# Optimization experiments

Measured on AMD Instinct MI355X. Metric: run time of the kernel, lower is better.

Reference implementation:

```python
import jax, jax.numpy as jnp
import numpy as np

H = 32        # query heads
D = 128       # head size
HID = H * D   # 4096
B = 4
S = 1024
T = B * S
NSLOTS = 16384
THETA = 10000.0


def _rope(x, cos, sin):
    # x: [T, ..., D]; cos/sin: [T, D//2] -> broadcast over head dims
    half = x.shape[-1] // 2
    while cos.ndim < x.ndim:
        cos = cos[:, None]
        sin = sin[:, None]
    x1, x2 = x[..., :half], x[..., half:]
    return jnp.concatenate([x1 * cos - x2 * sin, x2 * cos + x1 * sin], axis=-1)


def setup_inputs() -> dict:
    key = jax.random.key(0)
    ks = jax.random.split(key, 6)
    hidden_states = jax.random.normal(ks[0], (T, HID), jnp.float32)
    # rotary tables from real positions (repeat per sequence in the batch)
    pos = jnp.tile(jnp.arange(S, dtype=jnp.float32), B)          # [T]
    inv_freq = 1.0 / (THETA ** (jnp.arange(0, D, 2, dtype=jnp.float32) / D))  # [D/2]
    ang = pos[:, None] * inv_freq[None, :]                        # [T, D/2]
    cos, sin = jnp.cos(ang), jnp.sin(ang)
    qkv_w = jax.random.normal(ks[1], (HID, HID + 2 * D), jnp.float32) * 0.02
    qkv_b = jax.random.normal(ks[2], (HID + 2 * D,), jnp.float32) * 0.02
    dense_w = jax.random.normal(ks[3], (HID, HID), jnp.float32) * 0.02
    dense_b = jax.random.normal(ks[4], (HID,), jnp.float32) * 0.02
    k_cache = jnp.zeros((NSLOTS, D), jnp.float32)
    v_cache = jnp.zeros((NSLOTS, D), jnp.float32)
    slots = jnp.arange(T, dtype=jnp.int32)
    return {"hidden_states": hidden_states, "cos": cos, "sin": sin,
            "k_cache": k_cache, "v_cache": v_cache,
            "qkv_w": qkv_w, "qkv_b": qkv_b, "dense_w": dense_w,
            "dense_b": dense_b, "slots": slots, "batch_size": B}


def reference(hidden_states, cos, sin, k_cache, v_cache,
              qkv_w, qkv_b, dense_w, dense_b, slots, batch_size):
    scale = D ** -0.5
    qkv = hidden_states @ qkv_w + qkv_b                  # [T, H*D + 2D]
    q = qkv[:, :HID].reshape(T, H, D)                    # [T,H,D]
    kv = qkv[:, HID:].reshape(T, 2, D)                   # MQA: 1 kv head
    k, v = kv[:, 0], kv[:, 1]                            # [T,D]
    q = _rope(q, cos, sin)
    k = _rope(k, cos, sin)
    # KV-cache scatter store
    k_cache = k_cache.at[slots].set(k)
    v_cache = v_cache.at[slots].set(v)
    # prefill varlen causal attention (uniform lengths -> [B,S] layout)
    qb = q.reshape(batch_size, S, H, D)
    kb = k.reshape(batch_size, S, D)
    vb = v.reshape(batch_size, S, D)
    scores = jnp.einsum('bqhd,bkd->bhqk', qb, kb) * scale
    causal = jnp.tril(jnp.ones((S, S), bool))
    scores = jnp.where(causal[None, None], scores, jnp.float32(-1e30))
    probs = jax.nn.softmax(scores, axis=-1)
    attn = jnp.einsum('bhqk,bkd->bqhd', probs, vb).reshape(T, HID)
    out = attn @ dense_w + dense_b                       # [T, HID]
    return out, k_cache, v_cache
```

## Files before the change

kernel.cpp:

```cpp
#include <hip/hip_runtime.h>

#define H_   32
#define D_   128
#define HID_ 4096
#define B_   4
#define S_   1024
#define T_   4096
#define NSLOTS_ 16384
#define NQKV_ 4352

typedef __attribute__((ext_vector_type(8))) __bf16 bf16x8;
typedef __attribute__((ext_vector_type(4))) __bf16 bf16x4;
typedef __attribute__((ext_vector_type(4))) float  f32x4;

__device__ __forceinline__ void gld_lds16(const __bf16* g, __bf16* l)
{
    __builtin_amdgcn_global_load_lds(
        (const __attribute__((address_space(1))) void*)g,
        (__attribute__((address_space(3))) void*)l, 16, 0, 0);
}

__device__ __forceinline__ bf16x8 ds_read_b128a(const __bf16* p)
{
    bf16x8 r;
    unsigned a = (unsigned)(size_t)(const __attribute__((address_space(3))) __bf16*)p;
    asm volatile("ds_read_b128 %0, %1" : "=&v"(r) : "v"(a));
    return r;
}

__global__ __launch_bounds__(256) void cast_bf16_kernel(
    const float* __restrict__ in, __bf16* __restrict__ out, int n4)
{
    int i = blockIdx.x * 256 + threadIdx.x;
    if (i < n4) {
        f32x4 v = ((const f32x4*)in)[i];
        bf16x4 o;
        o[0] = (__bf16)v[0]; o[1] = (__bf16)v[1];
        o[2] = (__bf16)v[2]; o[3] = (__bf16)v[3];
        ((bf16x4*)out)[i] = o;
    }
}

__global__ __launch_bounds__(256) void transpose_cast_kernel(
    const float* __restrict__ in, __bf16* __restrict__ out, int R, int C)
{
    __shared__ float tile[32][33];
    int c0 = blockIdx.x * 32, r0 = blockIdx.y * 32;
    int tx = threadIdx.x;
    int ty = threadIdx.y;
#pragma unroll
    for (int j = 0; j < 32; j += 8)
        tile[ty + j][tx] = in[(size_t)(r0 + ty + j) * C + c0 + tx];
    __syncthreads();
#pragma unroll
    for (int j = 0; j < 32; j += 8)
        out[(size_t)(c0 + ty + j) * R + r0 + tx] = (__bf16)tile[tx][ty + j];
}


#define SB()    __builtin_amdgcn_sched_barrier(0)
#define BAR()   __builtin_amdgcn_s_barrier()
#define LGKM0() asm volatile("s_waitcnt lgkmcnt(0)" ::: "memory")

#define LOAD_A(MH, KK)                                                          \
    _Pragma("unroll")                                                           \
    for (int m = 0; m < 4; ++m)                                                 \
        afr[m] = ds_read_b128a(&lds[buf][KK][(wm * 128 + ((MH)*4 + m) * 16 + col) * 32 + pbE]);

#define MFMA_QUAD(MH, KK)                                                       \
    __builtin_amdgcn_s_setprio(1);                                              \
    _Pragma("unroll")                                                           \
    for (int m = 0; m < 4; ++m) {                                               \
        _Pragma("unroll")                                                       \
        for (int n = 0; n < 4; ++n)                                             \
            acc[(MH)*4 + m][n] = __builtin_amdgcn_mfma_f32_16x16x32_bf16(       \
                afr[m], bfr[KK][n], acc[(MH)*4 + m][n], 0, 0, 0);               \
    }                                                                           \
    __builtin_amdgcn_s_setprio(0);

__global__ __launch_bounds__(512, 2) void gemm256_kernel(
    const __bf16* __restrict__ A, const __bf16* __restrict__ Bt,
    const float* __restrict__ bias, float* __restrict__ C,
    int M, int N, int K)
{
    __shared__ __bf16 lds[2][4][8192];

    const int tid  = threadIdx.x;
    const int lane = tid & 63;
    const int wave = tid >> 6;
    const int wm   = wave >> 2;
    const int wn   = wave & 3;
    const int col  = lane & 15;
    const int quad = lane >> 4;
    const int pbE  = (quad ^ ((lane >> 1) & 3)) * 8;
    const int bm   = blockIdx.y * 256;
    const int bn   = blockIdx.x * 256;
    const int nk   = K >> 6;
    const int nitems = nk << 2;

    const int sR = wave * 32 + (lane >> 2);
    const int sb = ((lane & 3) ^ ((lane >> 3) & 3)) * 8;
    const __bf16* gA = A  + (size_t)(bm + sR) * K + sb;
    const __bf16* gB = Bt + (size_t)(bn + sR) * K + sb;

    f32x4 acc[8][4];
#pragma unroll
    for (int m = 0; m < 8; ++m)
#pragma unroll
        for (int n = 0; n < 4; ++n)
#pragma unroll
            for (int r = 0; r < 4; ++r) acc[m][n][r] = 0.f;

    auto stage = [&](int idx) {
        if (idx >= nitems) return;
        const int j   = idx >> 2;
        const int sel = idx & 3;
        const int reg = sel ^ 2;
        const __bf16* g = (sel & 2) ? gA : gB;
        const size_t koff = (size_t)j * 64 + (size_t)(sel & 1) * 32;
        __bf16* l = &lds[j & 1][reg][wave * 1024];
        gld_lds16(g + koff, l);
        gld_lds16(g + koff + (size_t)16 * K, l + 512);
    };

    stage(0); stage(1); stage(2); stage(3);
    asm volatile("s_waitcnt vmcnt(4)" ::: "memory");
    stage(4); stage(5); stage(6);
    asm volatile("s_waitcnt vmcnt(6)" ::: "memory");
    BAR();
    SB();

    for (int k = 0; k < nk; ++k) {
        const int buf = k & 1;
        bf16x8 bfr[2][4];
        bf16x8 afr[4];

#pragma unroll
        for (int kk = 0; kk < 2; ++kk)
#pragma unroll
            for (int n = 0; n < 4; ++n)
                bfr[kk][n] = ds_read_b128a(&lds[buf][2 + kk][(wn * 64 + n * 16 + col) * 32 + pbE]);
        LOAD_A(0, 0)
        stage(4 * k + 7);
        SB(); BAR(); LGKM0(); SB();
        MFMA_QUAD(0, 0)
        SB(); BAR(); SB();

        LOAD_A(1, 0)
        stage(4 * k + 8);
        SB(); BAR(); LGKM0(); SB();
        MFMA_QUAD(1, 0)
        SB(); BAR(); SB();

        LOAD_A(0, 1)
        stage(4 * k + 9);
        SB(); BAR(); LGKM0(); SB();
        MFMA_QUAD(0, 1)
        SB(); BAR(); SB();

        LOAD_A(1, 1)
        stage(4 * k + 10);
        SB(); BAR(); LGKM0(); SB();
        MFMA_QUAD(1, 1)
        SB();
        if (k < nk - 2) asm volatile("s_waitcnt vmcnt(6)" ::: "memory");
        else            asm volatile("s_waitcnt vmcnt(0)" ::: "memory");
        BAR();
        SB();
    }

#pragma unroll
    for (int m = 0; m < 8; ++m) {
#pragma unroll
        for (int n = 0; n < 4; ++n) {
            const int r0 = bm + wm * 128 + m * 16 + quad * 4;
            const int c0 = bn + wn * 64 + n * 16 + col;
            const float bv = bias[c0];
#pragma unroll
            for (int r = 0; r < 4; ++r)
                C[(size_t)(r0 + r) * N + c0] = acc[m][n][r] + bv;
        }
    }
}

__global__ __launch_bounds__(256) void rope_scatter_kernel(
    const float* __restrict__ qkv, const float* __restrict__ cosb,
    const float* __restrict__ sinb, const int* __restrict__ slots,
    __bf16* __restrict__ q16, __bf16* __restrict__ k16, __bf16* __restrict__ v16,
    float* __restrict__ kcache, float* __restrict__ vcache)
{
    const int t = blockIdx.x;
    const int tid = threadIdx.x;
    const float* row = qkv + (size_t)t * NQKV_;
    const float* cr = cosb + (size_t)t * 64;
    const float* sr = sinb + (size_t)t * 64;
    const int slot = slots[t];

#pragma unroll
    for (int i = 0; i < 8; ++i) {
        int p = tid + 256 * i;
        int h = p >> 6;
        int d = p & 63;
        float x1 = row[h * 128 + d];
        float x2 = row[h * 128 + 64 + d];
        float c = cr[d], s = sr[d];
        q16[(size_t)t * HID_ + h * 128 + d]      = (__bf16)(x1 * c - x2 * s);
        q16[(size_t)t * HID_ + h * 128 + 64 + d] = (__bf16)(x2 * c + x1 * s);
    }
    if (tid < 64) {
        int d = tid;
        float x1 = row[HID_ + d];
        float x2 = row[HID_ + 64 + d];
        float c = cr[d], s = sr[d];
        float o1 = x1 * c - x2 * s;
        float o2 = x2 * c + x1 * s;
        kcache[(size_t)slot * D_ + d]      = o1;
        kcache[(size_t)slot * D_ + 64 + d] = o2;
        k16[(size_t)t * D_ + d]      = (__bf16)o1;
        k16[(size_t)t * D_ + 64 + d] = (__bf16)o2;
    }
    if (tid < 128) {
        float v = row[HID_ + 128 + tid];
        vcache[(size_t)slot * D_ + tid] = v;
        v16[(size_t)t * D_ + tid] = (__bf16)v;
    }
}

__global__ __launch_bounds__(256) void attn_kernel(
    const __bf16* __restrict__ Q, const __bf16* __restrict__ Kc,
    const __bf16* __restrict__ Vc, __bf16* __restrict__ O)
{
    __shared__ __bf16 sK[64][136];
    __shared__ __bf16 sVt[128][72];
    __shared__ __bf16 sP[4][32][72];

    const int h  = blockIdx.y;
    const int b  = blockIdx.z;
    const int tid = threadIdx.x, lane = tid & 63, wave = tid >> 6;
    const int col = lane & 15, quad = lane >> 4;
    const int tbase = b * S_;
    const float scale = 0.08838834764831845f;

    for (int half = 0; half < 2; ++half) {
        const int qt = half ? (7 - blockIdx.x) : blockIdx.x;
        const int qb = qt * 128;

        bf16x8 aq[2][4];
#pragma unroll
        for (int mt = 0; mt < 2; ++mt)
#pragma unroll
            for (int ks = 0; ks < 4; ++ks)
                aq[mt][ks] = *(const bf16x8*)&Q[(size_t)(tbase + qb + wave * 32 + mt * 16 + col) * HID_
                                                + h * 128 + ks * 32 + quad * 8];

        f32x4 o[2][8];
#pragma unroll
        for (int mt = 0; mt < 2; ++mt)
#pragma unroll
            for (int nd = 0; nd < 8; ++nd)
#pragma unroll
                for (int r = 0; r < 4; ++r) o[mt][nd][r] = 0.f;
        float m_i[2][4], l_i[2][4];
#pragma unroll
        for (int mt = 0; mt < 2; ++mt)
#pragma unroll
            for (int r = 0; r < 4; ++r) { m_i[mt][r] = -3.0e38f; l_i[mt][r] = 0.f; }

        const int ntiles = qt * 2 + 2;
        for (int kt = 0; kt < ntiles; ++kt) {
            const int kb = kt * 64;
            __syncthreads();
#pragma unroll
            for (int i = 0; i < 4; ++i) {
                int c = tid + i * 256;
                int srow = c >> 4;
                int d0 = (c & 15) * 8;
                *(uint4*)&sK[srow][d0] = *(const uint4*)&Kc[(size_t)(tbase + kb + srow) * D_ + d0];
            }
#pragma unroll
            for (int i = 0; i < 4; ++i) {
                int c = tid + i * 256;
                int srow = c & 63;
                int d0 = (c >> 6) * 8;
                bf16x8 v = *(const bf16x8*)&Vc[(size_t)(tbase + kb + srow) * D_ + d0];
#pragma unroll
                for (int j = 0; j < 8; ++j) sVt[d0 + j][srow] = v[j];
            }
            __syncthreads();

            f32x4 sc[2][4];
#pragma unroll
            for (int mt = 0; mt < 2; ++mt)
#pragma unroll
                for (int nt = 0; nt < 4; ++nt)
#pragma unroll
                    for (int r = 0; r < 4; ++r) sc[mt][nt][r] = 0.f;
#pragma unroll
            for (int ks = 0; ks < 4; ++ks) {
                bf16x8 bk[4];
#pragma unroll
                for (int nt = 0; nt < 4; ++nt)
                    bk[nt] = *(const bf16x8*)&sK[nt * 16 + col][ks * 32 + quad * 8];
#pragma unroll
                for (int mt = 0; mt < 2; ++mt)
#pragma unroll
                    for (int nt = 0; nt < 4; ++nt)
                        sc[mt][nt] = __builtin_amdgcn_mfma_f32_16x16x32_bf16(
                            aq[mt][ks], bk[nt], sc[mt][nt], 0, 0, 0);
            }

#pragma unroll
            for (int mt = 0; mt < 2; ++mt) {
#pragma unroll
                for (int r = 0; r < 4; ++r) {
                    int qrow = qb + wave * 32 + mt * 16 + quad * 4 + r;
#pragma unroll
                    for (int nt = 0; nt < 4; ++nt) {
                        float v = sc[mt][nt][r] * scale;
                        int kcol = kb + nt * 16 + col;
                        sc[mt][nt][r] = (kcol > qrow) ? -3.0e38f : v;
                    }
                    float mx = sc[mt][0][r];
#pragma unroll
                    for (int nt = 1; nt < 4; ++nt) mx = fmaxf(mx, sc[mt][nt][r]);
#pragma unroll
                    for (int x = 1; x < 16; x <<= 1) mx = fmaxf(mx, __shfl_xor(mx, x, 64));
                    float mnew = fmaxf(m_i[mt][r], mx);
                    float alpha = __expf(m_i[mt][r] - mnew);
                    m_i[mt][r] = mnew;
                    float rs = 0.f;
#pragma unroll
                    for (int nt = 0; nt < 4; ++nt) {
                        float p = __expf(sc[mt][nt][r] - mnew);
                        sc[mt][nt][r] = p;
                        rs += p;
                    }
#pragma unroll
                    for (int x = 1; x < 16; x <<= 1) rs += __shfl_xor(rs, x, 64);
                    l_i[mt][r] = l_i[mt][r] * alpha + rs;
#pragma unroll
                    for (int nd = 0; nd < 8; ++nd) o[mt][nd][r] *= alpha;
                }
            }

#pragma unroll
            for (int mt = 0; mt < 2; ++mt)
#pragma unroll
                for (int nt = 0; nt < 4; ++nt)
#pragma unroll
                    for (int r = 0; r < 4; ++r)
                        sP[wave][mt * 16 + quad * 4 + r][nt * 16 + col] = (__bf16)sc[mt][nt][r];

#pragma unroll
            for (int ks2 = 0; ks2 < 2; ++ks2) {
                bf16x8 ap[2];
#pragma unroll
                for (int mt = 0; mt < 2; ++mt)
                    ap[mt] = *(const bf16x8*)&sP[wave][mt * 16 + col][ks2 * 32 + quad * 8];
#pragma unroll
                for (int nd = 0; nd < 8; ++nd) {
                    bf16x8 bv = *(const bf16x8*)&sVt[nd * 16 + col][ks2 * 32 + quad * 8];
#pragma unroll
                    for (int mt = 0; mt < 2; ++mt)
                        o[mt][nd] = __builtin_amdgcn_mfma_f32_16x16x32_bf16(
                            ap[mt], bv, o[mt][nd], 0, 0, 0);
                }
            }
        }

#pragma unroll
        for (int mt = 0; mt < 2; ++mt) {
#pragma unroll
            for (int r = 0; r < 4; ++r) {
                int t = tbase + qb + wave * 32 + mt * 16 + quad * 4 + r;
                float inv_l = 1.f / l_i[mt][r];
#pragma unroll
                for (int nd = 0; nd < 8; ++nd)
                    O[(size_t)t * HID_ + h * 128 + nd * 16 + col] = (__bf16)(o[mt][nd][r] * inv_l);
            }
        }
    }
}

extern "C" void kernel_launch(void* const* d_in, const int* in_sizes, int n_in,
                              void* d_out, int out_size, void* d_ws, size_t ws_size,
                              hipStream_t stream)
{
    const float* hidden  = (const float*)d_in[0];
    const float* cosb    = (const float*)d_in[1];
    const float* sinb    = (const float*)d_in[2];
    const float* kc_in   = (const float*)d_in[3];
    const float* vc_in   = (const float*)d_in[4];
    const float* qkv_w   = (const float*)d_in[5];
    const float* qkv_b   = (const float*)d_in[6];
    const float* dense_w = (const float*)d_in[7];
    const float* dense_b = (const float*)d_in[8];
    const int*   slots   = (const int*)d_in[9];

    float* out    = (float*)d_out;
    float* kc_out = out + (size_t)T_ * HID_;
    float* vc_out = kc_out + (size_t)NSLOTS_ * D_;

    char* ws = (char*)d_ws;
    __bf16* A16 = (__bf16*)(ws);
    __bf16* W1T = (__bf16*)(ws + 33554432);
    float*  QKV = (float*)(ws + 69206016);
    __bf16* W2T = (__bf16*)(ws + 69206016);
    __bf16* Q16 = (__bf16*)d_out;
    __bf16* K16 = (__bf16*)((char*)d_out + 33554432);
    __bf16* V16 = (__bf16*)((char*)d_out + 34603008);

    cast_bf16_kernel<<<(T_ * HID_ / 4 + 255) / 256, 256, 0, stream>>>(hidden, A16, T_ * HID_ / 4);
    transpose_cast_kernel<<<dim3(NQKV_ / 32, HID_ / 32), dim3(32, 8), 0, stream>>>(qkv_w, W1T, HID_, NQKV_);
    gemm256_kernel<<<dim3(NQKV_ / 256, T_ / 256), 512, 0, stream>>>(A16, W1T, qkv_b, QKV, T_, NQKV_, HID_);
    hipMemcpyAsync(kc_out, kc_in, (size_t)NSLOTS_ * D_ * 4, hipMemcpyDeviceToDevice, stream);
    hipMemcpyAsync(vc_out, vc_in, (size_t)NSLOTS_ * D_ * 4, hipMemcpyDeviceToDevice, stream);
    rope_scatter_kernel<<<T_, 256, 0, stream>>>(QKV, cosb, sinb, slots, Q16, K16, V16, kc_out, vc_out);
    transpose_cast_kernel<<<dim3(HID_ / 32, HID_ / 32), dim3(32, 8), 0, stream>>>(dense_w, W2T, HID_, HID_);
    attn_kernel<<<dim3(4, H_, B_), 256, 0, stream>>>(Q16, K16, V16, A16);
    gemm256_kernel<<<dim3(HID_ / 256, T_ / 256), 512, 0, stream>>>(A16, W2T, dense_b, out, T_, HID_, HID_);
}
```

Baseline: 734.4 us.

## Software-pipeline LDS fragment reads against MFMA in GEMM main loop

```diff
diff --git a/kernel.cpp b/kernel.cpp
--- a/kernel.cpp
+++ b/kernel.cpp
@@ -60,21 +60,15 @@
 
 #define SB()    __builtin_amdgcn_sched_barrier(0)
 #define BAR()   __builtin_amdgcn_s_barrier()
-#define LGKM0() asm volatile("s_waitcnt lgkmcnt(0)" ::: "memory")
-
-#define LOAD_A(MH, KK)                                                          \
-    _Pragma("unroll")                                                           \
-    for (int m = 0; m < 4; ++m)                                                 \
-        afr[m] = ds_read_b128a(&lds[buf][KK][(wm * 128 + ((MH)*4 + m) * 16 + col) * 32 + pbE]);
-
-#define MFMA_QUAD(MH, KK)                                                       \
+
+#define MFMA4(MH, AFR, BFR)                                                     \
     __builtin_amdgcn_s_setprio(1);                                              \
     _Pragma("unroll")                                                           \
     for (int m = 0; m < 4; ++m) {                                               \
         _Pragma("unroll")                                                       \
         for (int n = 0; n < 4; ++n)                                             \
             acc[(MH)*4 + m][n] = __builtin_amdgcn_mfma_f32_16x16x32_bf16(       \
-                afr[m], bfr[KK][n], acc[(MH)*4 + m][n], 0, 0, 0);               \
+                AFR[m], BFR[n], acc[(MH)*4 + m][n], 0, 0, 0);                   \
     }                                                                           \
     __builtin_amdgcn_s_setprio(0);
 
@@ -123,50 +117,66 @@
         gld_lds16(g + koff + (size_t)16 * K, l + 512);
     };
 
+    auto rdA = [&](int bf, int kk, int mh, bf16x8* dst) {
+#pragma unroll
+        for (int m = 0; m < 4; ++m)
+            dst[m] = ds_read_b128a(&lds[bf][kk][(wm * 128 + (mh * 4 + m) * 16 + col) * 32 + pbE]);
+    };
+    auto rdB = [&](int bf, int kk, bf16x8* dst) {
+#pragma unroll
+        for (int n = 0; n < 4; ++n)
+            dst[n] = ds_read_b128a(&lds[bf][2 + kk][(wn * 64 + n * 16 + col) * 32 + pbE]);
+    };
+
+    bf16x8 a_cur[4], a_nxt[4], b0[4], b1[4];
+
     stage(0); stage(1); stage(2); stage(3);
-    asm volatile("s_waitcnt vmcnt(4)" ::: "memory");
     stage(4); stage(5); stage(6);
-    asm volatile("s_waitcnt vmcnt(6)" ::: "memory");
+    asm volatile("s_waitcnt vmcnt(8)" ::: "memory");
     BAR();
     SB();
+    rdA(0, 0, 0, a_cur);
+    rdB(0, 0, b0);
+    SB();
 
     for (int k = 0; k < nk; ++k) {
         const int buf = k & 1;
-        bf16x8 bfr[2][4];
-        bf16x8 afr[4];
-
-#pragma unroll
-        for (int kk = 0; kk < 2; ++kk)
-#pragma unroll
-            for (int n = 0; n < 4; ++n)
-                bfr[kk][n] = ds_read_b128a(&lds[buf][2 + kk][(wn * 64 + n * 16 + col) * 32 + pbE]);
-        LOAD_A(0, 0)
+
+        rdA(buf, 0, 1, a_nxt);
+        rdB(buf, 1, b1);
         stage(4 * k + 7);
-        SB(); BAR(); LGKM0(); SB();
-        MFMA_QUAD(0, 0)
+        SB();
+        asm volatile("s_waitcnt lgkmcnt(8)" ::: "memory"); SB();
+        MFMA4(0, a_cur, b0)
+        SB();
+        if (k < nk - 2) asm volatile("s_waitcnt vmcnt(8)" ::: "memory");
+        else            asm volatile("s_waitcnt vmcnt(0)" ::: "memory");
+        BAR(); SB();
+
+        rdA(buf, 1, 0, a_cur);
+        stage(4 * k + 8);
+        SB();
+        asm volatile("s_waitcnt lgkmcnt(4)" ::: "memory"); SB();
+        MFMA4(1, a_nxt, b0)
         SB(); BAR(); SB();
 
-        LOAD_A(1, 0)
-        stage(4 * k + 8);
-        SB(); BAR(); LGKM0(); SB();
-        MFMA_QUAD(1, 0)
-        SB(); BAR(); SB();
-
-        LOAD_A(0, 1)
+        rdA(buf, 1, 1, a_nxt);
         stage(4 * k + 9);
-        SB(); BAR(); LGKM0(); SB();
-        MFMA_QUAD(0, 1)
-        SB(); BAR(); SB();
-
-        LOAD_A(1, 1)
-        stage(4 * k + 10);
-        SB(); BAR(); LGKM0(); SB();
-        MFMA_QUAD(1, 1)
+        SB();
+        asm volatile("s_waitcnt lgkmcnt(4)" ::: "memory"); SB();
+        MFMA4(0, a_cur, b1)
         SB();
         if (k < nk - 2) asm volatile("s_waitcnt vmcnt(6)" ::: "memory");
         else            asm volatile("s_waitcnt vmcnt(0)" ::: "memory");
-        BAR();
-        SB();
+        BAR(); SB();
+
+        rdA(buf ^ 1, 0, 0, a_cur);
+        rdB(buf ^ 1, 0, b0);
+        stage(4 * k + 10);
+        SB();
+        asm volatile("s_waitcnt lgkmcnt(8)" ::: "memory"); SB();
+        MFMA4(1, a_nxt, b1)
+        SB(); BAR(); SB();
     }
 
 #pragma unroll
```

Result: no change. 734.1 us (-0.0%).
